# Optimization experiments

Measured on AMD Instinct MI355X. Metric: run time of the kernel, lower is better.

Reference implementation:

```python
import jax, jax.numpy as jnp
from jax import lax
import numpy as np

CODE_DIM = 256
CODE_SIZE = 1024
BETA = 0.25


def _conv2d(x, w, b, stride, pad):
    # x: NCHW, w: OIHW (pytorch Conv2d layout)
    y = lax.conv_general_dilated(x, w, (stride, stride), [(pad, pad), (pad, pad)],
                                 dimension_numbers=('NCHW', 'OIHW', 'NCHW'))
    return y + b[None, :, None, None]


def _conv_transpose2d(x, w, b, stride, pad):
    # w: pytorch ConvTranspose2d layout [in, out, kh, kw]
    kh, kw = w.shape[2], w.shape[3]
    wf = jnp.flip(w, (2, 3)).transpose(1, 0, 2, 3)  # -> OIHW with spatial flip
    y = lax.conv_general_dilated(x, wf, (1, 1),
                                 [(kh - 1 - pad, kh - 1 - pad), (kw - 1 - pad, kw - 1 - pad)],
                                 lhs_dilation=(stride, stride),
                                 dimension_numbers=('NCHW', 'OIHW', 'NCHW'))
    return y + b[None, :, None, None]


def setup_inputs() -> dict:
    key = jax.random.key(0)
    ks = jax.random.split(key, 14)
    f32 = jnp.float32

    def p(k, shape, s=0.05):
        return jax.random.normal(k, shape, f32) * s

    return {
        'x': jax.random.normal(ks[0], (64, 1, 128, 128), f32),
        'enc_w1': p(ks[1], (64, 1, 5, 5)), 'enc_b1': jnp.zeros((64,), f32),
        'enc_w2': p(ks[2], (64, 64, 5, 5)), 'enc_b2': jnp.zeros((64,), f32),
        'enc_w3': p(ks[3], (CODE_DIM, 64, 5, 5)), 'enc_b3': jnp.zeros((CODE_DIM,), f32),
        'codebook': p(ks[4], (CODE_SIZE, CODE_DIM)),
        'dec_w1': p(ks[5], (CODE_DIM, 64, 4, 4)), 'dec_b1': jnp.zeros((64,), f32),
        'dec_w2': p(ks[6], (64, 64, 4, 4)), 'dec_b2': jnp.zeros((64,), f32),
        'dec_w3': p(ks[7], (1, 64, 3, 3)), 'dec_b3': jnp.zeros((1,), f32),
    }


def reference(x, enc_w1, enc_b1, enc_w2, enc_b2, enc_w3, enc_b3, codebook,
              dec_w1, dec_b1, dec_w2, dec_b2, dec_w3, dec_b3):
    # ---- encoder ----
    z = jax.nn.relu(_conv2d(x, enc_w1, enc_b1, 2, 2))
    z = jax.nn.relu(_conv2d(z, enc_w2, enc_b2, 1, 2))
    z = _conv2d(z, enc_w3, enc_b3, 2, 2)  # [B, D, H/4, W/4]

    # ---- quantize (eval mode: no EMA buffer updates) ----
    b, c, h, w = z.shape
    flat = z.transpose(0, 2, 3, 1).reshape(-1, c)  # [BHW, D]
    # ||z||^2 - 2 z.W^T + ||w||^2
    dists = ((flat ** 2).sum(axis=1, keepdims=True)
             - 2.0 * flat @ codebook.T
             + (codebook ** 2).sum(axis=1)[None, :])  # [BHW, K]
    idx = jnp.argmin(dists, axis=1)
    e = codebook[idx].reshape(b, h, w, c).transpose(0, 3, 1, 2)  # [B, D, h, w]
    e_st = lax.stop_gradient(e - z) + z  # straight-through

    # ---- decoder ----
    y = jax.nn.relu(_conv_transpose2d(e_st, dec_w1, dec_b1, 2, 1))
    y = jax.nn.relu(_conv_transpose2d(y, dec_w2, dec_b2, 2, 1))
    x_tilde = jnp.tanh(_conv2d(y, dec_w3, dec_b3, 1, 1))

    diff = jnp.mean((z - lax.stop_gradient(e)) ** 2)
    return x_tilde, diff
```

## Files before the change

kernel.cpp:

```cpp
#include <hip/hip_runtime.h>

typedef _Float16 f16;
typedef _Float16 f16x8 __attribute__((ext_vector_type(8)));
typedef _Float16 f16x4 __attribute__((ext_vector_type(4)));
typedef _Float16 h2 __attribute__((ext_vector_type(2)));
typedef float f32x4 __attribute__((ext_vector_type(4)));
typedef unsigned short u16;
typedef unsigned int u32;

#define DEVI __device__ __forceinline__

DEVI u16 f2h(float f) { f16 h = (f16)f; return __builtin_bit_cast(u16, h); }
DEVI float h2f(u16 u) { f16 h = __builtin_bit_cast(f16, u); return (float)h; }

__launch_bounds__(256)
__global__ void prep_wconv_k(const float* __restrict__ src, u16* __restrict__ dst, int nf_sh) {
    int i = blockIdx.x * 256 + threadIdx.x;
    int j = i & 7, lane = (i >> 3) & 63;
    int q = i >> 9;
    int f = q & ((1 << nf_sh) - 1); q >>= nf_sh;
    int pl = q & 1; q >>= 1;
    int icc = q & 1; int tap = q >> 1;
    int oc = (f << 4) + (lane & 15);
    int ic = icc * 32 + ((lane >> 4) << 3) + j;
    float w = src[(oc * 64 + ic) * 25 + tap];
    if (pl == 0) dst[i] = f2h(w);
    else         dst[i] = f2h((w - h2f(f2h(w))) * 4096.f);
}
__launch_bounds__(256)
__global__ void prep_wdec_k(const float* __restrict__ src, u16* __restrict__ dst, int icc_sh) {
    int i = blockIdx.x * 256 + threadIdx.x;
    int j = i & 7, lane = (i >> 3) & 63;
    int f = (i >> 9) & 3;
    int q = i >> 11;
    int icc = q & ((1 << icc_sh) - 1); int tap = q >> icc_sh;
    int oc = (f << 4) + (lane & 15);
    int ic = icc * 32 + ((lane >> 4) << 3) + j;
    dst[i] = f2h(src[(ic * 64 + oc) * 16 + tap]);
}
__launch_bounds__(256)
__global__ void prep_cb_k(const float* __restrict__ cb, u16* __restrict__ dst) {
    int i = blockIdx.x * 256 + threadIdx.x;
    int j = i & 7, lane = (i >> 3) & 63;
    int f = (i >> 9) & 63;
    int q = i >> 15;
    int pl = q & 1; int ks = q >> 1;
    int n = (f << 4) + (lane & 15);
    int k = ks * 32 + ((lane >> 4) << 3) + j;
    float w = cb[n * 256 + k];
    if (pl == 0) dst[i] = f2h(w);
    else         dst[i] = f2h((w - h2f(f2h(w))) * 4096.f);
}
__launch_bounds__(256)
__global__ void prep_cbn_k(const float* __restrict__ cb, float* __restrict__ cbn) {
    int row = blockIdx.x * 256 + threadIdx.x;
    float s = 0.f;
    for (int c = 0; c < 256; c += 4) {
        f32x4 v = *(const f32x4*)&cb[row * 256 + c];
        s = fmaf(v.x, v.x, s); s = fmaf(v.y, v.y, s);
        s = fmaf(v.z, v.z, s); s = fmaf(v.w, v.w, s);
    }
    cbn[row] = s;
}

__launch_bounds__(256)
__global__ void conv1_k(const float* __restrict__ x, const float* __restrict__ w,
                        const float* __restrict__ b, u16* __restrict__ oh, u16* __restrict__ ol) {
    __shared__ float wl[25 * 64];
    __shared__ float bl[64];
    int t = threadIdx.x;
    for (int i = t; i < 1600; i += 256) wl[(i % 25) * 64 + i / 25] = w[i];
    if (t < 64) bl[t] = b[t];
    __syncthreads();
    int p = blockIdx.x * 256 + t;
    int ox = p & 63, oy = (p >> 6) & 63, n = p >> 12;
    f32x4 acc[16];
    #pragma unroll
    for (int c = 0; c < 16; ++c) acc[c] = *(f32x4*)&bl[c * 4];
    for (int dy = 0; dy < 5; ++dy) {
        int iy = 2 * oy - 2 + dy;
        if ((unsigned)iy >= 128u) continue;
        for (int dx = 0; dx < 5; ++dx) {
            int ix = 2 * ox - 2 + dx;
            if ((unsigned)ix >= 128u) continue;
            float v = x[(n * 128 + iy) * 128 + ix];
            const float* wp = &wl[(dy * 5 + dx) * 64];
            #pragma unroll
            for (int c = 0; c < 16; ++c) {
                f32x4 w4 = *(const f32x4*)&wp[c * 4];
                acc[c].x = fmaf(v, w4.x, acc[c].x); acc[c].y = fmaf(v, w4.y, acc[c].y);
                acc[c].z = fmaf(v, w4.z, acc[c].z); acc[c].w = fmaf(v, w4.w, acc[c].w);
            }
        }
    }
    #pragma unroll
    for (int c = 0; c < 16; ++c) {
        ushort4 uh, ul;
        float vv[4] = {acc[c].x, acc[c].y, acc[c].z, acc[c].w};
        u16 rh[4], rl[4];
        #pragma unroll
        for (int k = 0; k < 4; ++k) {
            float v = fmaxf(vv[k], 0.f);
            f16 hh = (f16)v;
            rh[k] = __builtin_bit_cast(u16, hh);
            rl[k] = f2h((v - (float)hh) * 4096.f);
        }
        uh.x = rh[0]; uh.y = rh[1]; uh.z = rh[2]; uh.w = rh[3];
        ul.x = rl[0]; ul.y = rl[1]; ul.z = rl[2]; ul.w = rl[3];
        *(ushort4*)&oh[p * 64 + c * 4] = uh;
        *(ushort4*)&ol[p * 64 + c * 4] = ul;
    }
}

template<int S, int OCT, int NI, bool RELU>
__launch_bounds__(256)
__global__ void conv5_k(const u16* __restrict__ Ah_g, const u16* __restrict__ Al_g,
                        const u16* __restrict__ wBf, const float* __restrict__ bias,
                        u16* __restrict__ Oh, u16* __restrict__ Ol,
                        int IH, int IW, int OH, int OW) {
    constexpr int PATCH = 7 * S + 5;
    constexpr int NPIX = PATCH * PATCH;
    constexpr int NPAIR = (NPIX + 1) / 2;
    constexpr int PLSZ = NPAIR * 64;
    constexpr int NF = OCT / 16;
    constexpr int BN = NI * 32;
    constexpr int OCB = OCT / BN;
    __shared__ u16 patch[2 * PLSZ];

    int t = threadIdx.x, l = t & 63, wv = t >> 6;
    int wm = wv >> 1, wn = wv & 1, g = l >> 4;

    int bi = blockIdx.x;
    int ocb = bi % OCB; int rest = bi / OCB;
    int tw = OW >> 3, th = OH >> 3;
    int txi = rest % tw; rest /= tw;
    int tyi = rest % th; int n = rest / th;
    int iy0 = S * (tyi << 3) - 2, ix0 = S * (txi << 3) - 2;

    int ppb[2];
    #pragma unroll
    for (int mi = 0; mi < 2; ++mi) {
        int m = wm * 32 + mi * 16 + (l & 15);
        int py = m >> 3, px = m & 7;
        ppb[mi] = (S * py) * PATCH + S * px;
    }

    f32x4 acc0[2][NI], acc1[2][NI];
    f32x4 z4 = {0.f, 0.f, 0.f, 0.f};
    #pragma unroll
    for (int mi = 0; mi < 2; ++mi)
        #pragma unroll
        for (int ni = 0; ni < NI; ++ni) { acc0[mi][ni] = z4; acc1[mi][ni] = z4; }

    int tap0 = bi % 25;
    int dy0 = tap0 / 5, dx0 = tap0 - 5 * dy0;
    int iccr = bi & 1;
    int fg = ocb * (BN / 16) + wn * NI;
    const size_t tstride = (size_t)(4 * NF) * 512;

    for (int icci = 0; icci < 2; ++icci) {
        int icc = icci ^ iccr;
        __syncthreads();
        for (int i = t; i < NPIX * 8; i += 256) {
            int c = i & 3; int r2 = i >> 2;
            int pl = (r2 >= NPIX); int pp = r2 - pl * NPIX;
            int py = pp / PATCH, px = pp - py * PATCH;
            int iy = iy0 + py, ix = ix0 + px;
            uint4 v = make_uint4(0u, 0u, 0u, 0u);
            if ((unsigned)iy < (unsigned)IH && (unsigned)ix < (unsigned)IW)
                v = *(const uint4*)&(pl ? Al_g : Ah_g)[(((n * IH + iy) * IW + ix)) * 64 + icc * 32 + c * 8];
            int P = pp >> 1, r = pp & 1;
            *(uint4*)&patch[pl * PLSZ + (P << 6) + (((P + (c << 1) + r) & 7) << 3)] = v;
        }
        __syncthreads();

        const u16* pB = wBf + (size_t)((tap0 * 4 + icc * 2) * NF + fg) * 512 + l * 8;
        f16x8 Bh0[NI], Bl0[NI], Bh1[NI], Bl1[NI];
        #pragma unroll
        for (int ni = 0; ni < NI; ++ni) {
            Bh0[ni] = *(const f16x8*)&pB[ni * 512];
            Bl0[ni] = *(const f16x8*)&pB[(NF + ni) * 512];
        }
        int tap = tap0, dy = dy0, dx = dx0;
        int tadd = dy0 * PATCH + dx0;
        for (int tapi = 0; tapi < 25; ++tapi) {
            const u16* pBn = (tap == 24) ? (pB - 24 * tstride) : (pB + tstride);
            if (tapi < 24) {
                #pragma unroll
                for (int ni = 0; ni < NI; ++ni) {
                    Bh1[ni] = *(const f16x8*)&pBn[ni * 512];
                    Bl1[ni] = *(const f16x8*)&pBn[(NF + ni) * 512];
                }
            }
            #pragma unroll
            for (int mi = 0; mi < 2; ++mi) {
                int pp = ppb[mi] + tadd;
                int P = pp >> 1, r = pp & 1;
                int offs = (P << 6) + (((P + (g << 1) + r) & 7) << 3);
                f16x8 ah = *(const f16x8*)&patch[offs];
                f16x8 al = *(const f16x8*)&patch[PLSZ + offs];
                #pragma unroll
                for (int ni = 0; ni < NI; ++ni) {
                    acc0[mi][ni] = __builtin_amdgcn_mfma_f32_16x16x32_f16(ah, Bh0[ni], acc0[mi][ni], 0, 0, 0);
                    acc1[mi][ni] = __builtin_amdgcn_mfma_f32_16x16x32_f16(ah, Bl0[ni], acc1[mi][ni], 0, 0, 0);
                    acc1[mi][ni] = __builtin_amdgcn_mfma_f32_16x16x32_f16(al, Bh0[ni], acc1[mi][ni], 0, 0, 0);
                }
            }
            #pragma unroll
            for (int ni = 0; ni < NI; ++ni) { Bh0[ni] = Bh1[ni]; Bl0[ni] = Bl1[ni]; }
            pB = pBn;
            tap = (tap == 24) ? 0 : tap + 1;
            if (tap == 0) { dy = 0; dx = 0; tadd = 0; }
            else {
                dx++; tadd++;
                if (dx == 5) { dx = 0; dy++; tadd += PATCH - 5; }
            }
        }
    }
    #pragma unroll
    for (int mi = 0; mi < 2; ++mi)
        #pragma unroll
        for (int ni = 0; ni < NI; ++ni) {
            int oc = ocb * BN + wn * (NI * 16) + ni * 16 + (l & 15);
            float bv = bias[oc];
            #pragma unroll
            for (int reg = 0; reg < 4; ++reg) {
                float v = acc0[mi][ni][reg] + acc1[mi][ni][reg] * (1.f / 4096.f) + bv;
                if (RELU) v = fmaxf(v, 0.f);
                int pix = wm * 32 + mi * 16 + g * 4 + reg;
                int oy = (tyi << 3) + (pix >> 3), ox = (txi << 3) + (pix & 7);
                int idx = ((n * OH + oy) * OW + ox) * OCT + oc;
                f16 hh = (f16)v;
                Oh[idx] = __builtin_bit_cast(u16, hh);
                Ol[idx] = f2h((v - (float)hh) * 4096.f);
            }
        }
}

__launch_bounds__(256, 2)
__global__ void quant_k(const u16* __restrict__ zh, const u16* __restrict__ zl,
                        const u16* __restrict__ cbf, const float* __restrict__ cbn,
                        const float* __restrict__ cb, u16* __restrict__ e,
                        float* __restrict__ diff) {
    __shared__ u16 Bbuf[2 * 32 * 512];
    __shared__ float cbn_l[1024];
    __shared__ float zn_l[128];
    __shared__ float bd_l[128];
    __shared__ int   wi_l[128];

    int t = threadIdx.x, l = t & 63, wv = t >> 6, g = l >> 4;
    int bi = blockIdx.x;
    int row0 = bi << 7;

    {
        f32x4 v = *(const f32x4*)&cbn[t * 4];
        *(f32x4*)&cbn_l[t * 4] = v;
    }

    f16x8 Ah[2][8], Al[2][8];
    int rbase = row0 + wv * 32 + (l & 15);
    #pragma unroll
    for (int mi = 0; mi < 2; ++mi)
        #pragma unroll
        for (int ks = 0; ks < 8; ++ks) {
            size_t off = (size_t)(rbase + mi * 16) * 256 + ks * 32 + g * 8;
            Ah[mi][ks] = *(const f16x8*)&zh[off];
            Al[mi][ks] = *(const f16x8*)&zl[off];
        }

    #pragma unroll
    for (int mi = 0; mi < 2; ++mi) {
        float s = 0.f;
        #pragma unroll
        for (int ks = 0; ks < 8; ++ks)
            #pragma unroll
            for (int j = 0; j < 8; ++j) {
                float v = (float)Ah[mi][ks][j] + (float)Al[mi][ks][j] * (1.f / 4096.f);
                s = fmaf(v, v, s);
            }
        s += __shfl_xor(s, 16);
        s += __shfl_xor(s, 32);
        if (g == 0) zn_l[wv * 32 + mi * 16 + (l & 15)] = s;
    }

    float rd[8]; int rc[8];
    #pragma unroll
    for (int s = 0; s < 8; ++s) { rd[s] = 1e30f; rc[s] = 0; }

    int fi = wv * 8;
    {
        int no0 = bi & 31;
        #pragma unroll
        for (int q = 0; q < 8; ++q) {
            int f2 = fi + q;
            int ks = f2 >> 2, pl = (f2 >> 1) & 1, nf = f2 & 1;
            f16x8 v = *(const f16x8*)&cbf[(size_t)(((ks * 2 + pl) * 64) + no0 * 2 + nf) * 512 + l * 8];
            *(uint4*)&Bbuf[(size_t)f2 * 512 + l * 8] = __builtin_bit_cast(uint4, v);
        }
    }
    __syncthreads();

    for (int noi = 0; noi < 32; ++noi) {
        int b = noi & 1;
        int no_cur = (noi + bi) & 31;

        f16x8 pf[8];
        if (noi < 31) {
            int no_n = (noi + 1 + bi) & 31;
            #pragma unroll
            for (int q = 0; q < 8; ++q) {
                int f2 = fi + q;
                int ks = f2 >> 2, pl = (f2 >> 1) & 1, nf = f2 & 1;
                pf[q] = *(const f16x8*)&cbf[(size_t)(((ks * 2 + pl) * 64) + no_n * 2 + nf) * 512 + l * 8];
            }
        }

        f32x4 acc0[2][2], acc1[2][2];
        f32x4 z4 = {0.f, 0.f, 0.f, 0.f};
        #pragma unroll
        for (int mi = 0; mi < 2; ++mi)
            #pragma unroll
            for (int nf = 0; nf < 2; ++nf) { acc0[mi][nf] = z4; acc1[mi][nf] = z4; }

        #pragma unroll
        for (int ks = 0; ks < 8; ++ks) {
            const u16* bb = &Bbuf[(size_t)(b * 32 + ks * 4) * 512 + l * 8];
            f16x8 Bh0 = *(const f16x8*)&bb[0 * 512];
            f16x8 Bh1 = *(const f16x8*)&bb[1 * 512];
            f16x8 Bl0 = *(const f16x8*)&bb[2 * 512];
            f16x8 Bl1 = *(const f16x8*)&bb[3 * 512];
            #pragma unroll
            for (int mi = 0; mi < 2; ++mi) {
                acc0[mi][0] = __builtin_amdgcn_mfma_f32_16x16x32_f16(Ah[mi][ks], Bh0, acc0[mi][0], 0, 0, 0);
                acc0[mi][1] = __builtin_amdgcn_mfma_f32_16x16x32_f16(Ah[mi][ks], Bh1, acc0[mi][1], 0, 0, 0);
                acc1[mi][0] = __builtin_amdgcn_mfma_f32_16x16x32_f16(Ah[mi][ks], Bl0, acc1[mi][0], 0, 0, 0);
                acc1[mi][0] = __builtin_amdgcn_mfma_f32_16x16x32_f16(Al[mi][ks], Bh0, acc1[mi][0], 0, 0, 0);
                acc1[mi][1] = __builtin_amdgcn_mfma_f32_16x16x32_f16(Ah[mi][ks], Bl1, acc1[mi][1], 0, 0, 0);
                acc1[mi][1] = __builtin_amdgcn_mfma_f32_16x16x32_f16(Al[mi][ks], Bh1, acc1[mi][1], 0, 0, 0);
            }
        }

        #pragma unroll
        for (int nf = 0; nf < 2; ++nf) {
            int col = no_cur * 32 + nf * 16 + (l & 15);
            float cn = cbn_l[col];
            #pragma unroll
            for (int mi = 0; mi < 2; ++mi)
                #pragma unroll
                for (int reg = 0; reg < 4; ++reg) {
                    float d = cn - 2.f * (acc0[mi][nf][reg] + acc1[mi][nf][reg] * (1.f / 4096.f));
                    int slot = mi * 4 + reg;
                    if (d < rd[slot] || (d == rd[slot] && col < rc[slot])) { rd[slot] = d; rc[slot] = col; }
                }
        }

        if (noi < 31) {
            #pragma unroll
            for (int q = 0; q < 8; ++q)
                *(uint4*)&Bbuf[(size_t)((1 - b) * 32 + fi + q) * 512 + l * 8] = __builtin_bit_cast(uint4, pf[q]);
        }
        __syncthreads();
    }

    #pragma unroll
    for (int step = 1; step < 16; step <<= 1) {
        #pragma unroll
        for (int s = 0; s < 8; ++s) {
            float od = __shfl_xor(rd[s], step);
            int ocl = __shfl_xor(rc[s], step);
            if (od < rd[s] || (od == rd[s] && ocl < rc[s])) { rd[s] = od; rc[s] = ocl; }
        }
    }
    if ((l & 15) == 0) {
        #pragma unroll
        for (int s = 0; s < 8; ++s) {
            int mi = s >> 2, reg = s & 3;
            int row = wv * 32 + mi * 16 + g * 4 + reg;
            bd_l[row] = rd[s]; wi_l[row] = rc[s];
        }
    }
    __syncthreads();
    if (t < 64) {
        float dval = (zn_l[t] + bd_l[t]) + (zn_l[t + 64] + bd_l[t + 64]);
        #pragma unroll
        for (int step = 1; step < 64; step <<= 1) dval += __shfl_xor(dval, step);
        if (t == 0) atomicAdd(diff, dval * (1.f / 16777216.f));
    }
    __syncthreads();
    for (int r = 0; r < 128; ++r) {
        int wi = wi_l[r];
        e[(size_t)(row0 + r) * 256 + t] = f2h(cb[wi * 256 + t]);
    }
}

template<int ICT>
__launch_bounds__(256)
__global__ void deconv4_k(const u16* __restrict__ in, const u16* __restrict__ wdf,
                          const float* __restrict__ bias, u16* __restrict__ out,
                          int IH, int IW) {
    constexpr int RST = 40;
    constexpr int ICC = ICT / 32;
    constexpr int PLSZ = 81 * RST;
    __shared__ u16 patch[PLSZ];

    int t = threadIdx.x, l = t & 63, wv = t >> 6;
    int wm = wv >> 1, wn = wv & 1, g = l >> 4;

    int bi = blockIdx.x;
    int par = bi & 3; int ry = par >> 1, rx = par & 1;
    int rest = bi >> 2;
    int tw = IW >> 3, th = IH >> 3;
    int txi = rest % tw; rest /= tw;
    int tyi = rest % th; int n = rest / th;
    int a0 = tyi << 3, b0 = txi << 3;
    int by0 = ry ? 0 : -1, bx0 = rx ? 0 : -1;
    int OH = IH << 1, OW = IW << 1;

    int pb0[2];
    #pragma unroll
    for (int mi = 0; mi < 2; ++mi) {
        int m = wm * 32 + mi * 16 + (l & 15);
        int pa = m >> 3, pb_ = m & 7;
        pb0[mi] = (pa * 9 + pb_) * RST + g * 8;
    }

    f32x4 acc[2][2];
    f32x4 z4 = {0.f, 0.f, 0.f, 0.f};
    #pragma unroll
    for (int mi = 0; mi < 2; ++mi)
        #pragma unroll
        for (int ni = 0; ni < 2; ++ni) acc[mi][ni] = z4;

    auto ldB = [&](int icc, int tt, f16x8* B) {
        int tty = tt >> 1, ttx = tt & 1;
        int ky = 1 - ry + 2 * tty, kx = 1 - rx + 2 * ttx;
        int tap = ky * 4 + kx;
        #pragma unroll
        for (int ni = 0; ni < 2; ++ni)
            B[ni] = *(const f16x8*)&wdf[(size_t)((tap * ICC + icc) * 4 + wn * 2 + ni) * 512 + l * 8];
    };

    f16x8 B0[2], B1[2];
    {
        int icc0 = (bi >> 2) & (ICC - 1);
        ldB(icc0, bi & 3, B0);
    }

    for (int icci = 0; icci < ICC; ++icci) {
        int icc = (icci + (bi >> 2)) & (ICC - 1);
        __syncthreads();
        for (int i = t; i < 324; i += 256) {
            int c = i & 3; int pp = i >> 2;
            int pr = pp / 9, pc = pp - pr * 9;
            int ar = a0 + by0 + pr, ac = b0 + bx0 + pc;
            uint4 v = make_uint4(0u, 0u, 0u, 0u);
            if ((unsigned)ar < (unsigned)IH && (unsigned)ac < (unsigned)IW)
                v = *(const uint4*)&in[((n * IH + ar) * IW + ac) * ICT + icc * 32 + c * 8];
            *(uint4*)&patch[(pr * 9 + pc) * RST + c * 8] = v;
        }
        __syncthreads();
        #pragma unroll
        for (int tti = 0; tti < 4; ++tti) {
            int tt = (tti + bi) & 3;
            if (!(icci == ICC - 1 && tti == 3)) {
                int nicci = (tti == 3) ? icci + 1 : icci;
                int ntti = (tti == 3) ? 0 : tti + 1;
                int nicc = (nicci + (bi >> 2)) & (ICC - 1);
                ldB(nicc, (ntti + bi) & 3, B1);
            }
            int tty = tt >> 1, ttx = tt & 1;
            int shift = ((1 - tty) * 9 + (1 - ttx)) * RST;
            #pragma unroll
            for (int mi = 0; mi < 2; ++mi) {
                f16x8 a = *(const f16x8*)&patch[pb0[mi] + shift];
                #pragma unroll
                for (int ni = 0; ni < 2; ++ni)
                    acc[mi][ni] = __builtin_amdgcn_mfma_f32_16x16x32_f16(a, B0[ni], acc[mi][ni], 0, 0, 0);
            }
            B0[0] = B1[0]; B0[1] = B1[1];
        }
    }
    #pragma unroll
    for (int mi = 0; mi < 2; ++mi)
        #pragma unroll
        for (int ni = 0; ni < 2; ++ni) {
            int oc = wn * 32 + ni * 16 + (l & 15);
            float bv = bias[oc];
            #pragma unroll
            for (int reg = 0; reg < 4; ++reg) {
                float v = fmaxf(acc[mi][ni][reg] + bv, 0.f);
                int pix = wm * 32 + mi * 16 + g * 4 + reg;
                int oy = ((a0 + (pix >> 3)) << 1) + ry;
                int ox = ((b0 + (pix & 7)) << 1) + rx;
                out[((n * OH + oy) * OW + ox) * 64 + oc] = f2h(v);
            }
        }
}

__launch_bounds__(256)
__global__ void conv3x3_tanh_k(const u16* __restrict__ in, const float* __restrict__ w,
                               const float* __restrict__ b, float* __restrict__ out) {
    __shared__ u16 tile[18 * 18 * 72];
    __shared__ u32 wpk[288];
    int t = threadIdx.x;
    int bi = blockIdx.x;
    int n = bi >> 6;
    int tile6 = bi & 63;
    int ty0 = (tile6 >> 3) << 4, tx0 = (tile6 & 7) << 4;

    for (int i = t; i < 288; i += 256) {
        int tap = i >> 5, icp = i & 31;
        h2 p;
        p.x = (f16)w[(2 * icp) * 9 + tap];
        p.y = (f16)w[(2 * icp + 1) * 9 + tap];
        wpk[tap * 32 + icp] = __builtin_bit_cast(u32, p);
    }
    for (int i = t; i < 2592; i += 256) {
        int ch = i & 7, pix = i >> 3;
        int pr = pix / 18, pc = pix - pr * 18;
        int gy = ty0 - 1 + pr, gx = tx0 - 1 + pc;
        uint4 v = make_uint4(0u, 0u, 0u, 0u);
        if ((unsigned)gy < 128u && (unsigned)gx < 128u)
            v = *(const uint4*)&in[(((n << 7) + gy) * 128 + gx) * 64 + ch * 8];
        *(uint4*)&tile[pix * 72 + ch * 8] = v;
    }
    __syncthreads();

    int ty = t >> 4, tx = t & 15;
    float acc = b[0];
    #pragma unroll
    for (int dy = 0; dy < 3; ++dy) {
        #pragma unroll
        for (int dx = 0; dx < 3; ++dx) {
            int base = ((ty + dy) * 18 + (tx + dx)) * 72;
            const u32* wp = &wpk[(dy * 3 + dx) * 32];
            #pragma unroll
            for (int c8 = 0; c8 < 8; ++c8) {
                uint4 v = *(const uint4*)&tile[base + c8 * 8];
                acc = __builtin_amdgcn_fdot2(__builtin_bit_cast(h2, v.x),
                        __builtin_bit_cast(h2, wp[c8 * 4 + 0]), acc, false);
                acc = __builtin_amdgcn_fdot2(__builtin_bit_cast(h2, v.y),
                        __builtin_bit_cast(h2, wp[c8 * 4 + 1]), acc, false);
                acc = __builtin_amdgcn_fdot2(__builtin_bit_cast(h2, v.z),
                        __builtin_bit_cast(h2, wp[c8 * 4 + 2]), acc, false);
                acc = __builtin_amdgcn_fdot2(__builtin_bit_cast(h2, v.w),
                        __builtin_bit_cast(h2, wp[c8 * 4 + 3]), acc, false);
            }
        }
    }
    int oy = ty0 + ty, ox = tx0 + tx;
    out[(n << 14) + (oy << 7) + ox] = tanhf(acc);
}

extern "C" void kernel_launch(void* const* d_in, const int* in_sizes, int n_in,
                              void* d_out, int out_size, void* d_ws, size_t ws_size,
                              hipStream_t stream) {
    (void)in_sizes; (void)n_in; (void)out_size; (void)ws_size;
    const float* x   = (const float*)d_in[0];
    const float* ew1 = (const float*)d_in[1];
    const float* eb1 = (const float*)d_in[2];
    const float* ew2 = (const float*)d_in[3];
    const float* eb2 = (const float*)d_in[4];
    const float* ew3 = (const float*)d_in[5];
    const float* eb3 = (const float*)d_in[6];
    const float* cb  = (const float*)d_in[7];
    const float* dw1 = (const float*)d_in[8];
    const float* db1 = (const float*)d_in[9];
    const float* dw2 = (const float*)d_in[10];
    const float* db2 = (const float*)d_in[11];
    const float* dw3 = (const float*)d_in[12];
    const float* db3 = (const float*)d_in[13];
    float* out = (float*)d_out;

    u16* ws = (u16*)d_ws;
    u16* a1h = ws;             u16* a1l = ws + 16777216;
    u16* zh  = ws;             u16* zl  = ws + 16777216;
    u16* a2h = ws + 33554432;  u16* a2l = ws + 50331648;
    u16* e   = ws + 33554432;
    u16* y1  = ws + 67108864;
    u16* y2  = ws;
    u16* wBf2 = ws + 83886080;
    u16* wBf3 = wBf2 + 204800;
    u16* wd1f = wBf3 + 819200;
    u16* wd2f = wd1f + 262144;
    u16* cbf  = wd2f + 65536;
    float* cbn = (float*)(cbf + 524288);

    hipMemsetAsync(out + 1048576, 0, 4, stream);

    prep_wconv_k<<<800, 256, 0, stream>>>(ew2, wBf2, 2);
    prep_wconv_k<<<3200, 256, 0, stream>>>(ew3, wBf3, 4);
    prep_wdec_k<<<1024, 256, 0, stream>>>(dw1, wd1f, 3);
    prep_wdec_k<<<256, 256, 0, stream>>>(dw2, wd2f, 1);
    prep_cb_k<<<2048, 256, 0, stream>>>(cb, cbf);
    prep_cbn_k<<<4, 256, 0, stream>>>(cb, cbn);

    conv1_k<<<1024, 256, 0, stream>>>(x, ew1, eb1, a1h, a1l);
    conv5_k<1, 64, 2, true><<<4096, 256, 0, stream>>>(a1h, a1l, wBf2, eb2, a2h, a2l, 64, 64, 64, 64);
    conv5_k<2, 256, 4, false><<<2048, 256, 0, stream>>>(a2h, a2l, wBf3, eb3, zh, zl, 64, 64, 32, 32);
    quant_k<<<512, 256, 0, stream>>>(zh, zl, cbf, cbn, cb, e, out + 1048576);
    deconv4_k<256><<<4096, 256, 0, stream>>>(e, wd1f, db1, y1, 32, 32);
    deconv4_k<64><<<16384, 256, 0, stream>>>(y1, wd2f, db2, y2, 64, 64);
    conv3x3_tanh_k<<<4096, 256, 0, stream>>>(y2, dw3, db3, out);
}
```

Measured before the change: 735.1 us.

## Precompute patch load offsets and prefetch LDS operands instead of weights in conv5

The conv5 kernel now computes the global and shared-memory offsets for patch staging once, before the channel-chunk loop, and reuses them for both chunks, so the per-chunk divisions and index math are dropped. The software pipeline changes to prefetch the next tap's LDS A-fragments, while the weight fragments for the current tap are loaded from global memory just before the MFMAs. This trades weight-load latency hiding for LDS-read latency hiding and uses more registers for the offset arrays.

```diff
diff --git a/kernel.cpp b/kernel.cpp
--- a/kernel.cpp
+++ b/kernel.cpp
@@ -125,6 +125,8 @@
     constexpr int NF = OCT / 16;
     constexpr int BN = NI * 32;
     constexpr int OCB = OCT / BN;
+    constexpr int NITER = (NPIX * 8 + 255) / 256;
+    constexpr int REM = NPIX * 8 - (NITER - 1) * 256;
     __shared__ u16 patch[2 * PLSZ];
 
     int t = threadIdx.x, l = t & 63, wv = t >> 6;
@@ -141,80 +143,106 @@
     #pragma unroll
     for (int mi = 0; mi < 2; ++mi) {
         int m = wm * 32 + mi * 16 + (l & 15);
-        int py = m >> 3, px = m & 7;
-        ppb[mi] = (S * py) * PATCH + S * px;
-    }
-
-    f32x4 acc0[2][NI], acc1[2][NI];
-    f32x4 z4 = {0.f, 0.f, 0.f, 0.f};
-    #pragma unroll
-    for (int mi = 0; mi < 2; ++mi)
-        #pragma unroll
-        for (int ni = 0; ni < NI; ++ni) { acc0[mi][ni] = z4; acc1[mi][ni] = z4; }
-
-    int tap0 = bi % 25;
-    int dy0 = tap0 / 5, dx0 = tap0 - 5 * dy0;
-    int iccr = bi & 1;
-    int fg = ocb * (BN / 16) + wn * NI;
-    const size_t tstride = (size_t)(4 * NF) * 512;
-
-    for (int icci = 0; icci < 2; ++icci) {
-        int icc = icci ^ iccr;
-        __syncthreads();
-        for (int i = t; i < NPIX * 8; i += 256) {
+        ppb[mi] = (S * (m >> 3)) * PATCH + S * (m & 7);
+    }
+
+    ptrdiff_t pd = Al_g - Ah_g;
+    int goff[NITER], loff[NITER];
+    #pragma unroll
+    for (int j = 0; j < NITER; ++j) {
+        goff[j] = -1; loff[j] = 0;
+        int i = t + j * 256;
+        if (j < NITER - 1 || i < NPIX * 8) {
             int c = i & 3; int r2 = i >> 2;
             int pl = (r2 >= NPIX); int pp = r2 - pl * NPIX;
             int py = pp / PATCH, px = pp - py * PATCH;
             int iy = iy0 + py, ix = ix0 + px;
-            uint4 v = make_uint4(0u, 0u, 0u, 0u);
+            int P = pp >> 1, r = pp & 1;
+            loff[j] = pl * PLSZ + (P << 6) + (((P + (c << 1) + r) & 7) << 3);
             if ((unsigned)iy < (unsigned)IH && (unsigned)ix < (unsigned)IW)
-                v = *(const uint4*)&(pl ? Al_g : Ah_g)[(((n * IH + iy) * IW + ix)) * 64 + icc * 32 + c * 8];
+                goff[j] = (((n * IH + iy) * IW + ix) << 6) + c * 8;
+        }
+    }
+
+    f32x4 acc0[2][NI], acc1[2][NI];
+    f32x4 z4 = {0.f, 0.f, 0.f, 0.f};
+    #pragma unroll
+    for (int mi = 0; mi < 2; ++mi)
+        #pragma unroll
+        for (int ni = 0; ni < NI; ++ni) { acc0[mi][ni] = z4; acc1[mi][ni] = z4; }
+
+    int tap0 = bi % 25;
+    int dy0 = tap0 / 5, dx0 = tap0 - 5 * dy0;
+    int tadd0 = dy0 * PATCH + dx0;
+    int iccr = bi & 1;
+    int fg = ocb * (BN / 16) + wn * NI;
+    const size_t tstride = (size_t)(4 * NF) * 512;
+
+    for (int icci = 0; icci < 2; ++icci) {
+        int icc = icci ^ iccr;
+        __syncthreads();
+        #pragma unroll
+        for (int j = 0; j < NITER; ++j) {
+            if (j < NITER - 1 || t < REM) {
+                uint4 v = make_uint4(0u, 0u, 0u, 0u);
+                int go = goff[j];
+                if (go >= 0) {
+                    const u16* gp = Ah_g + go + icc * 32;
+                    if (loff[j] >= PLSZ) gp += pd;
+                    v = *(const uint4*)gp;
+                }
+                *(uint4*)&patch[loff[j]] = v;
+            }
+        }
+        __syncthreads();
+
+        const u16* pB = wBf + (size_t)((tap0 * 4 + icc * 2) * NF + fg) * 512 + l * 8;
+        f16x8 ah0[2], al0[2], ah1[2], al1[2];
+        #pragma unroll
+        for (int mi = 0; mi < 2; ++mi) {
+            int pp = ppb[mi] + tadd0;
             int P = pp >> 1, r = pp & 1;
-            *(uint4*)&patch[pl * PLSZ + (P << 6) + (((P + (c << 1) + r) & 7) << 3)] = v;
-        }
-        __syncthreads();
-
-        const u16* pB = wBf + (size_t)((tap0 * 4 + icc * 2) * NF + fg) * 512 + l * 8;
-        f16x8 Bh0[NI], Bl0[NI], Bh1[NI], Bl1[NI];
-        #pragma unroll
-        for (int ni = 0; ni < NI; ++ni) {
-            Bh0[ni] = *(const f16x8*)&pB[ni * 512];
-            Bl0[ni] = *(const f16x8*)&pB[(NF + ni) * 512];
-        }
-        int tap = tap0, dy = dy0, dx = dx0;
-        int tadd = dy0 * PATCH + dx0;
+            int offs = (P << 6) + (((P + (g << 1) + r) & 7) << 3);
+            ah0[mi] = *(const f16x8*)&patch[offs];
+            al0[mi] = *(const f16x8*)&patch[PLSZ + offs];
+        }
+        int tap = tap0, dx = dx0, tadd = tadd0;
         for (int tapi = 0; tapi < 25; ++tapi) {
-            const u16* pBn = (tap == 24) ? (pB - 24 * tstride) : (pB + tstride);
+            int ntap, ndx, ntadd;
+            if (tap == 24) { ntap = 0; ndx = 0; ntadd = 0; }
+            else {
+                ntap = tap + 1; ndx = dx + 1; ntadd = tadd + 1;
+                if (ndx == 5) { ndx = 0; ntadd = tadd + (PATCH - 4); }
+            }
             if (tapi < 24) {
                 #pragma unroll
-                for (int ni = 0; ni < NI; ++ni) {
-                    Bh1[ni] = *(const f16x8*)&pBn[ni * 512];
-                    Bl1[ni] = *(const f16x8*)&pBn[(NF + ni) * 512];
+                for (int mi = 0; mi < 2; ++mi) {
+                    int pp = ppb[mi] + ntadd;
+                    int P = pp >> 1, r = pp & 1;
+                    int offs = (P << 6) + (((P + (g << 1) + r) & 7) << 3);
+                    ah1[mi] = *(const f16x8*)&patch[offs];
+                    al1[mi] = *(const f16x8*)&patch[PLSZ + offs];
                 }
             }
+            f16x8 Bh[NI], Bl[NI];
+            #pragma unroll
+            for (int ni = 0; ni < NI; ++ni) {
+                Bh[ni] = *(const f16x8*)&pB[ni * 512];
+                Bl[ni] = *(const f16x8*)&pB[(NF + ni) * 512];
+            }
             #pragma unroll
             for (int mi = 0; mi < 2; ++mi) {
-                int pp = ppb[mi] + tadd;
-                int P = pp >> 1, r = pp & 1;
-                int offs = (P << 6) + (((P + (g << 1) + r) & 7) << 3);
-                f16x8 ah = *(const f16x8*)&patch[offs];
-                f16x8 al = *(const f16x8*)&patch[PLSZ + offs];
                 #pragma unroll
                 for (int ni = 0; ni < NI; ++ni) {
-                    acc0[mi][ni] = __builtin_amdgcn_mfma_f32_16x16x32_f16(ah, Bh0[ni], acc0[mi][ni], 0, 0, 0);
-                    acc1[mi][ni] = __builtin_amdgcn_mfma_f32_16x16x32_f16(ah, Bl0[ni], acc1[mi][ni], 0, 0, 0);
-                    acc1[mi][ni] = __builtin_amdgcn_mfma_f32_16x16x32_f16(al, Bh0[ni], acc1[mi][ni], 0, 0, 0);
+                    acc0[mi][ni] = __builtin_amdgcn_mfma_f32_16x16x32_f16(ah0[mi], Bh[ni], acc0[mi][ni], 0, 0, 0);
+                    acc1[mi][ni] = __builtin_amdgcn_mfma_f32_16x16x32_f16(ah0[mi], Bl[ni], acc1[mi][ni], 0, 0, 0);
+                    acc1[mi][ni] = __builtin_amdgcn_mfma_f32_16x16x32_f16(al0[mi], Bh[ni], acc1[mi][ni], 0, 0, 0);
                 }
             }
             #pragma unroll
-            for (int ni = 0; ni < NI; ++ni) { Bh0[ni] = Bh1[ni]; Bl0[ni] = Bl1[ni]; }
-            pB = pBn;
-            tap = (tap == 24) ? 0 : tap + 1;
-            if (tap == 0) { dy = 0; dx = 0; tadd = 0; }
-            else {
-                dx++; tadd++;
-                if (dx == 5) { dx = 0; dy++; tadd += PATCH - 5; }
-            }
+            for (int mi = 0; mi < 2; ++mi) { ah0[mi] = ah1[mi]; al0[mi] = al1[mi]; }
+            pB = (tap == 24) ? (pB - 24 * tstride) : (pB + tstride);
+            tap = ntap; dx = ndx; tadd = ntadd;
         }
     }
     #pragma unroll
```

Result: faster. 720.6 us (-2.0%).

## Enlarge conv5 per-warp tiles to 4x4 MFMA blocks and remap block order

Applied to the files above, without the earlier changes.

The 5x5 conv kernel is restructured so each wave computes a 64-pixel by 64-channel tile (4x4 MFMA fragments). For conv2 this uses a 16x16 spatial tile with all output channels; for conv3 each wave handles a different 64-channel slice of an 8x8 tile. Launching fewer, larger blocks increases reuse of the shared-memory input patch and the weight fragments, which cuts redundant patch loads. The trade-offs are removing the register double-buffering of B weights and using many more accumulator registers, which can lower occupancy. Block indices in several kernels are also remapped with an XCD-style interleave so that neighbouring tiles share a die's L2.

```diff
diff --git a/kernel.cpp b/kernel.cpp
--- a/kernel.cpp
+++ b/kernel.cpp
@@ -112,50 +112,53 @@
     }
 }
 
-template<int S, int OCT, int NI, bool RELU>
+template<int S, int OCT, bool PARTOC, int TH, int TW, bool RELU>
 __launch_bounds__(256)
 __global__ void conv5_k(const u16* __restrict__ Ah_g, const u16* __restrict__ Al_g,
                         const u16* __restrict__ wBf, const float* __restrict__ bias,
                         u16* __restrict__ Oh, u16* __restrict__ Ol,
                         int IH, int IW, int OH, int OW) {
-    constexpr int PATCH = 7 * S + 5;
-    constexpr int NPIX = PATCH * PATCH;
+    constexpr int PATCH_H = S * (TH - 1) + 5;
+    constexpr int PATCH_W = S * (TW - 1) + 5;
+    constexpr int NPIX = PATCH_H * PATCH_W;
     constexpr int NPAIR = (NPIX + 1) / 2;
     constexpr int PLSZ = NPAIR * 64;
     constexpr int NF = OCT / 16;
-    constexpr int BN = NI * 32;
-    constexpr int OCB = OCT / BN;
     __shared__ u16 patch[2 * PLSZ];
 
-    int t = threadIdx.x, l = t & 63, wv = t >> 6;
-    int wm = wv >> 1, wn = wv & 1, g = l >> 4;
+    int t = threadIdx.x, l = t & 63, wv = t >> 6, g = l >> 4;
 
     int bi = blockIdx.x;
-    int ocb = bi % OCB; int rest = bi / OCB;
-    int tw = OW >> 3, th = OH >> 3;
+    int wlin = (bi & 7) * ((int)gridDim.x >> 3) + (bi >> 3);
+    int tw = OW / TW, th = OH / TH;
+    int rest = wlin;
     int txi = rest % tw; rest /= tw;
     int tyi = rest % th; int n = rest / th;
-    int iy0 = S * (tyi << 3) - 2, ix0 = S * (txi << 3) - 2;
-
-    int ppb[2];
-    #pragma unroll
-    for (int mi = 0; mi < 2; ++mi) {
-        int m = wm * 32 + mi * 16 + (l & 15);
-        int py = m >> 3, px = m & 7;
-        ppb[mi] = (S * py) * PATCH + S * px;
-    }
-
-    f32x4 acc0[2][NI], acc1[2][NI];
+    int iy0 = S * (tyi * TH) - 2, ix0 = S * (txi * TW) - 2;
+
+    int ppb[4];
+    #pragma unroll
+    for (int mi = 0; mi < 4; ++mi) {
+        if (PARTOC) {
+            int m = mi * 16 + (l & 15);
+            ppb[mi] = (S * (m >> 3)) * PATCH_W + S * (m & 7);
+        } else {
+            ppb[mi] = (S * (wv * 4 + mi)) * PATCH_W + S * (l & 15);
+        }
+    }
+
+    f32x4 acc0[4][4], acc1[4][4];
     f32x4 z4 = {0.f, 0.f, 0.f, 0.f};
     #pragma unroll
-    for (int mi = 0; mi < 2; ++mi)
-        #pragma unroll
-        for (int ni = 0; ni < NI; ++ni) { acc0[mi][ni] = z4; acc1[mi][ni] = z4; }
+    for (int mi = 0; mi < 4; ++mi)
+        #pragma unroll
+        for (int ni = 0; ni < 4; ++ni) { acc0[mi][ni] = z4; acc1[mi][ni] = z4; }
 
     int tap0 = bi % 25;
     int dy0 = tap0 / 5, dx0 = tap0 - 5 * dy0;
+    int tadd0 = dy0 * PATCH_W + dx0;
     int iccr = bi & 1;
-    int fg = ocb * (BN / 16) + wn * NI;
+    int fgbase = PARTOC ? (wv * 4) : 0;
     const size_t tstride = (size_t)(4 * NF) * 512;
 
     for (int icci = 0; icci < 2; ++icci) {
@@ -164,7 +167,7 @@
         for (int i = t; i < NPIX * 8; i += 256) {
             int c = i & 3; int r2 = i >> 2;
             int pl = (r2 >= NPIX); int pp = r2 - pl * NPIX;
-            int py = pp / PATCH, px = pp - py * PATCH;
+            int py = pp / PATCH_W, px = pp - py * PATCH_W;
             int iy = iy0 + py, ix = ix0 + px;
             uint4 v = make_uint4(0u, 0u, 0u, 0u);
             if ((unsigned)iy < (unsigned)IH && (unsigned)ix < (unsigned)IW)
@@ -174,61 +177,57 @@
         }
         __syncthreads();
 
-        const u16* pB = wBf + (size_t)((tap0 * 4 + icc * 2) * NF + fg) * 512 + l * 8;
-        f16x8 Bh0[NI], Bl0[NI], Bh1[NI], Bl1[NI];
-        #pragma unroll
-        for (int ni = 0; ni < NI; ++ni) {
-            Bh0[ni] = *(const f16x8*)&pB[ni * 512];
-            Bl0[ni] = *(const f16x8*)&pB[(NF + ni) * 512];
-        }
-        int tap = tap0, dy = dy0, dx = dx0;
-        int tadd = dy0 * PATCH + dx0;
+        const u16* pB = wBf + (size_t)((tap0 * 4 + icc * 2) * NF + fgbase) * 512 + l * 8;
+        int tap = tap0, dx = dx0, tadd = tadd0;
         for (int tapi = 0; tapi < 25; ++tapi) {
-            const u16* pBn = (tap == 24) ? (pB - 24 * tstride) : (pB + tstride);
-            if (tapi < 24) {
-                #pragma unroll
-                for (int ni = 0; ni < NI; ++ni) {
-                    Bh1[ni] = *(const f16x8*)&pBn[ni * 512];
-                    Bl1[ni] = *(const f16x8*)&pBn[(NF + ni) * 512];
-                }
-            }
-            #pragma unroll
-            for (int mi = 0; mi < 2; ++mi) {
+            f16x8 Bh[4], Bl[4];
+            #pragma unroll
+            for (int ni = 0; ni < 4; ++ni) {
+                Bh[ni] = *(const f16x8*)&pB[ni * 512];
+                Bl[ni] = *(const f16x8*)&pB[(NF + ni) * 512];
+            }
+            f16x8 ah[4], al[4];
+            #pragma unroll
+            for (int mi = 0; mi < 4; ++mi) {
                 int pp = ppb[mi] + tadd;
                 int P = pp >> 1, r = pp & 1;
                 int offs = (P << 6) + (((P + (g << 1) + r) & 7) << 3);
-                f16x8 ah = *(const f16x8*)&patch[offs];
-                f16x8 al = *(const f16x8*)&patch[PLSZ + offs];
+                ah[mi] = *(const f16x8*)&patch[offs];
+                al[mi] = *(const f16x8*)&patch[PLSZ + offs];
+            }
+            #pragma unroll
+            for (int mi = 0; mi < 4; ++mi)
                 #pragma unroll
-                for (int ni = 0; ni < NI; ++ni) {
-                    acc0[mi][ni] = __builtin_amdgcn_mfma_f32_16x16x32_f16(ah, Bh0[ni], acc0[mi][ni], 0, 0, 0);
-                    acc1[mi][ni] = __builtin_amdgcn_mfma_f32_16x16x32_f16(ah, Bl0[ni], acc1[mi][ni], 0, 0, 0);
-                    acc1[mi][ni] = __builtin_amdgcn_mfma_f32_16x16x32_f16(al, Bh0[ni], acc1[mi][ni], 0, 0, 0);
+                for (int ni = 0; ni < 4; ++ni) {
+                    acc0[mi][ni] = __builtin_amdgcn_mfma_f32_16x16x32_f16(ah[mi], Bh[ni], acc0[mi][ni], 0, 0, 0);
+                    acc1[mi][ni] = __builtin_amdgcn_mfma_f32_16x16x32_f16(ah[mi], Bl[ni], acc1[mi][ni], 0, 0, 0);
+                    acc1[mi][ni] = __builtin_amdgcn_mfma_f32_16x16x32_f16(al[mi], Bh[ni], acc1[mi][ni], 0, 0, 0);
                 }
-            }
-            #pragma unroll
-            for (int ni = 0; ni < NI; ++ni) { Bh0[ni] = Bh1[ni]; Bl0[ni] = Bl1[ni]; }
-            pB = pBn;
-            tap = (tap == 24) ? 0 : tap + 1;
-            if (tap == 0) { dy = 0; dx = 0; tadd = 0; }
+            pB = (tap == 24) ? (pB - 24 * tstride) : (pB + tstride);
+            if (tap == 24) { tap = 0; dx = 0; tadd = 0; }
             else {
-                dx++; tadd++;
-                if (dx == 5) { dx = 0; dy++; tadd += PATCH - 5; }
-            }
-        }
-    }
-    #pragma unroll
-    for (int mi = 0; mi < 2; ++mi)
-        #pragma unroll
-        for (int ni = 0; ni < NI; ++ni) {
-            int oc = ocb * BN + wn * (NI * 16) + ni * 16 + (l & 15);
+                tap++; dx++; tadd++;
+                if (dx == 5) { dx = 0; tadd += PATCH_W - 5; }
+            }
+        }
+    }
+    #pragma unroll
+    for (int mi = 0; mi < 4; ++mi)
+        #pragma unroll
+        for (int ni = 0; ni < 4; ++ni) {
+            int oc = fgbase * 16 + ni * 16 + (l & 15);
             float bv = bias[oc];
             #pragma unroll
             for (int reg = 0; reg < 4; ++reg) {
                 float v = acc0[mi][ni][reg] + acc1[mi][ni][reg] * (1.f / 4096.f) + bv;
                 if (RELU) v = fmaxf(v, 0.f);
-                int pix = wm * 32 + mi * 16 + g * 4 + reg;
-                int oy = (tyi << 3) + (pix >> 3), ox = (txi << 3) + (pix & 7);
+                int oy, ox;
+                if (PARTOC) {
+                    int pix = mi * 16 + g * 4 + reg;
+                    oy = tyi * TH + (pix >> 3); ox = txi * TW + (pix & 7);
+                } else {
+                    oy = tyi * TH + wv * 4 + mi; ox = txi * TW + g * 4 + reg;
+                }
                 int idx = ((n * OH + oy) * OW + ox) * OCT + oc;
                 f16 hh = (f16)v;
                 Oh[idx] = __builtin_bit_cast(u16, hh);
@@ -407,8 +406,9 @@
     int wm = wv >> 1, wn = wv & 1, g = l >> 4;
 
     int bi = blockIdx.x;
-    int par = bi & 3; int ry = par >> 1, rx = par & 1;
-    int rest = bi >> 2;
+    int wlin = (bi & 7) * ((int)gridDim.x >> 3) + (bi >> 3);
+    int par = wlin & 3; int ry = par >> 1, rx = par & 1;
+    int rest = wlin >> 2;
     int tw = IW >> 3, th = IH >> 3;
     int txi = rest % tw; rest /= tw;
     int tyi = rest % th; int n = rest / th;
@@ -504,8 +504,9 @@
     __shared__ u32 wpk[288];
     int t = threadIdx.x;
     int bi = blockIdx.x;
-    int n = bi >> 6;
-    int tile6 = bi & 63;
+    int wlin = (bi & 7) * ((int)gridDim.x >> 3) + (bi >> 3);
+    int n = wlin >> 6;
+    int tile6 = wlin & 63;
     int ty0 = (tile6 >> 3) << 4, tx0 = (tile6 & 7) << 4;
 
     for (int i = t; i < 288; i += 256) {
@@ -596,8 +597,8 @@
     prep_cbn_k<<<4, 256, 0, stream>>>(cb, cbn);
 
     conv1_k<<<1024, 256, 0, stream>>>(x, ew1, eb1, a1h, a1l);
-    conv5_k<1, 64, 2, true><<<4096, 256, 0, stream>>>(a1h, a1l, wBf2, eb2, a2h, a2l, 64, 64, 64, 64);
-    conv5_k<2, 256, 4, false><<<2048, 256, 0, stream>>>(a2h, a2l, wBf3, eb3, zh, zl, 64, 64, 32, 32);
+    conv5_k<1, 64, false, 16, 16, true><<<1024, 256, 0, stream>>>(a1h, a1l, wBf2, eb2, a2h, a2l, 64, 64, 64, 64);
+    conv5_k<2, 256, true, 8, 8, false><<<1024, 256, 0, stream>>>(a2h, a2l, wBf3, eb3, zh, zl, 64, 64, 32, 32);
     quant_k<<<512, 256, 0, stream>>>(zh, zl, cbf, cbn, cb, e, out + 1048576);
     deconv4_k<256><<<4096, 256, 0, stream>>>(e, wd1f, db1, y1, 32, 32);
     deconv4_k<64><<<16384, 256, 0, stream>>>(y1, wd2f, db2, y2, 64, 64);
```

After: 702.8 us. 4.4% less time.
